# Optimization experiments

Measured on AMD Instinct MI355X. Metric: run time of the kernel, lower is better.

The kernel has to match this reference:

```python
import jax, jax.numpy as jnp
import numpy as np

B, H, W, C = 4, 128, 128, 180
NH, WS = 6, 16
HD = C // NH
SCALE = HD ** -0.5
CONV_SCALE = 0.01
CR, SQ = 3, 30
HIDDEN = int(C * 4.0)


def setup_inputs() -> dict:
    key = jax.random.key(0)
    ks = iter(jax.random.split(key, 32))
    def rn(shape, s=0.02):
        return jax.random.normal(next(ks), shape, jnp.float32) * s
    return {
        "x": jax.random.normal(next(ks), (B, H * W, C), jnp.float32),
        "rpi": jax.random.randint(next(ks), (WS * WS, WS * WS), 0, (2 * WS - 1) ** 2),
        "attn_mask": jnp.zeros((1, 1, 1), jnp.int32),
        "triangular_masks": jnp.zeros((1,), jnp.int32),
        "h": H,
        "w": W,
        "norm1_g": jnp.ones((C,), jnp.float32), "norm1_b": jnp.zeros((C,), jnp.float32),
        "qkv_w": rn((C, 3 * C)), "qkv_b": jnp.zeros((3 * C,), jnp.float32),
        "rpb": rn(((2 * WS - 1) ** 2, NH)),
        "proj_w": rn((C, C)), "proj_b": jnp.zeros((C,), jnp.float32),
        "conv1_w": rn((3, 3, C, C // CR)), "conv1_b": jnp.zeros((C // CR,), jnp.float32),
        "conv2_w": rn((3, 3, C // CR, C)), "conv2_b": jnp.zeros((C,), jnp.float32),
        "ca1_w": rn((C, C // SQ)), "ca1_b": jnp.zeros((C // SQ,), jnp.float32),
        "ca2_w": rn((C // SQ, C)), "ca2_b": jnp.zeros((C,), jnp.float32),
        "norm2_g": jnp.ones((C,), jnp.float32), "norm2_b": jnp.zeros((C,), jnp.float32),
        "fc1_w": rn((C, HIDDEN)), "fc1_b": jnp.zeros((HIDDEN,), jnp.float32),
        "fc2_w": rn((HIDDEN, C)), "fc2_b": jnp.zeros((C,), jnp.float32),
    }


def _ln(x, g, b):
    mu = jnp.mean(x, -1, keepdims=True)
    var = jnp.var(x, -1, keepdims=True)
    return (x - mu) * jax.lax.rsqrt(var + 1e-5) * g + b


def _conv(x, w, b):
    y = jax.lax.conv_general_dilated(x, w, (1, 1), 'SAME',
                                     dimension_numbers=('NHWC', 'HWIO', 'NHWC'))
    return y + b


def _forward(x, norm1_g, norm1_b, qkv_w, qkv_b, rpb, proj_w, proj_b,
             conv1_w, conv1_b, conv2_w, conv2_b, ca1_w, ca1_b, ca2_w, ca2_b,
             norm2_g, norm2_b, fc1_w, fc1_b, fc2_w, fc2_b, rpi):
    b = x.shape[0]
    shortcut = x
    xn = _ln(x, norm1_g, norm1_b).reshape(b, H, W, C)
    # ---- CAB conv branch (conv3x3 -> GELU -> conv3x3 -> channel attention) ----
    y = _conv(xn, conv1_w, conv1_b)
    y = jax.nn.gelu(y, approximate=False)
    y = _conv(y, conv2_w, conv2_b)
    pooled = jnp.mean(y, axis=(1, 2))                      # (b, C) adaptive avg pool
    a = jax.nn.relu(pooled @ ca1_w + ca1_b)
    a = jax.nn.sigmoid(a @ ca2_w + ca2_b)
    conv_x = (y * a[:, None, None, :]).reshape(b, H * W, C)
    # ---- window partition (shift_size=0, triangular_flag=0) ----
    xw = xn.reshape(b, H // WS, WS, W // WS, WS, C)
    xw = xw.transpose(0, 1, 3, 2, 4, 5).reshape(-1, WS * WS, C)  # (b_, n, C)
    b_, n = xw.shape[0], WS * WS
    # ---- W-MSA with relative position bias ----
    qkv = (xw @ qkv_w + qkv_b).reshape(b_, n, 3, NH, HD).transpose(2, 0, 3, 1, 4)
    q, k, v = qkv[0] * SCALE, qkv[1], qkv[2]               # (b_, NH, n, HD)
    attn = jnp.einsum('bhnd,bhmd->bhnm', q, k)
    bias = rpb[rpi.reshape(-1)].reshape(n, n, NH).transpose(2, 0, 1)  # (NH, n, n)
    attn = jax.nn.softmax(attn + bias[None], axis=-1)
    out = jnp.einsum('bhnm,bhmd->bhnd', attn, v)
    out = out.transpose(0, 2, 1, 3).reshape(b_, n, C) @ proj_w + proj_b
    # ---- window reverse ----
    attn_x = out.reshape(b, H // WS, W // WS, WS, WS, C)
    attn_x = attn_x.transpose(0, 1, 3, 2, 4, 5).reshape(b, H * W, C)
    x = shortcut + attn_x + conv_x * CONV_SCALE
    # ---- MLP ----
    xn2 = _ln(x, norm2_g, norm2_b)
    m = jax.nn.gelu(xn2 @ fc1_w + fc1_b, approximate=False) @ fc2_w + fc2_b
    return x + m


def reference(x, rpi, attn_mask, triangular_masks, h, w,
              norm1_g, norm1_b, qkv_w, qkv_b, rpb, proj_w, proj_b,
              conv1_w, conv1_b, conv2_w, conv2_b, ca1_w, ca1_b, ca2_w, ca2_b,
              norm2_g, norm2_b, fc1_w, fc1_b, fc2_w, fc2_b):
    # attn_mask / triangular_masks unused: shift_size=0, triangular_flag=0.
    return _forward(x, norm1_g, norm1_b, qkv_w, qkv_b, rpb, proj_w, proj_b,
                    conv1_w, conv1_b, conv2_w, conv2_b, ca1_w, ca1_b, ca2_w, ca2_b,
                    norm2_g, norm2_b, fc1_w, fc1_b, fc2_w, fc2_b, rpi)
```

## Files before the change

kernel.cpp:

```cpp
#include <hip/hip_runtime.h>
#include <hip/hip_bf16.h>
#include <math.h>

typedef __hip_bfloat16 bf16;

#define B_    4
#define C_    180
#define ROWS_ 65536
#define NH_   6
#define HD_   30
#define NT_   256
#define CC_   60
#define HID_  720
#define ATT_SCALE 0.18257418583505536f

typedef short  short4v __attribute__((ext_vector_type(4)));
typedef short  short8v __attribute__((ext_vector_type(8)));
typedef __bf16 bf16x8  __attribute__((ext_vector_type(8)));
typedef float  f32x4   __attribute__((ext_vector_type(4)));

__device__ __forceinline__ float b2f(bf16 v){ return __bfloat162float(v); }
__device__ __forceinline__ bf16  f2b(float v){ return __float2bfloat16(v); }
__device__ __forceinline__ float ldf(const bf16* p){ return __bfloat162float(*p); }
__device__ __forceinline__ float ldf(const float* p){ return *p; }
__device__ __forceinline__ float gelu_f(float v){
    return 0.5f * v * (1.0f + erff(v * 0.70710678118654752440f));
}
__device__ __forceinline__ f32x4 mfma16(short8v a, short8v b, f32x4 c){
    return __builtin_amdgcn_mfma_f32_16x16x32_bf16(
        __builtin_bit_cast(bf16x8, a), __builtin_bit_cast(bf16x8, b), c, 0, 0, 0);
}
__device__ __forceinline__ short8v cat44(short4v lo, short4v hi){
    return short8v{lo[0],lo[1],lo[2],lo[3],hi[0],hi[1],hi[2],hi[3]};
}

__device__ __forceinline__ int inv_win(int r){
    int b = r >> 14, w6 = (r >> 8) & 63, t = r & 255;
    int py = ((w6 >> 3) << 4) + (t >> 4);
    int px = ((w6 & 7) << 4) + (t & 15);
    return (b << 14) + (py << 7) + px;
}

template<typename TIN>
__global__ __launch_bounds__(256) void ln_kernel(const TIN* __restrict__ xin,
        const float* __restrict__ gw, const float* __restrict__ gb,
        bf16* __restrict__ xn)
{
    int row  = blockIdx.x * 4 + (threadIdx.x >> 6);
    int lane = threadIdx.x & 63;
    const TIN* xp = xin + (size_t)row * C_;
    float v0 = ldf(xp + lane);
    float v1 = ldf(xp + lane + 64);
    float v2 = (lane < 52) ? ldf(xp + lane + 128) : 0.f;
    float s  = v0 + v1 + v2;
    float sq = v0*v0 + v1*v1 + v2*v2;
    for (int off = 32; off > 0; off >>= 1){
        s  += __shfl_xor(s,  off);
        sq += __shfl_xor(sq, off);
    }
    float mu  = s * (1.f / 180.f);
    float inv = rsqrtf(sq * (1.f / 180.f) - mu * mu + 1e-5f);
    size_t ro = (size_t)row * C_;
    #pragma unroll
    for (int e = 0; e < 3; e++){
        int c = lane + e * 64;
        if (c < C_){
            float v = (e == 0) ? v0 : (e == 1 ? v1 : v2);
            xn[ro + c] = f2b((v - mu) * inv * gw[c] + gb[c]);
        }
    }
}

__global__ __launch_bounds__(256) void twt_kernel(const float* __restrict__ w,
        bf16* __restrict__ bt, int K, int N, int KP, int NP)
{
    int idx = blockIdx.x * 256 + threadIdx.x;
    if (idx >= NP * KP) return;
    int n = idx / KP, k = idx % KP;
    float v = (n < N && k < K) ? w[(size_t)k * N + n] : 0.f;
    bt[idx] = f2b(v);
}
__global__ __launch_bounds__(256) void twc_kernel(const float* __restrict__ w,
        bf16* __restrict__ bt, int CIN, int N, int SEGP, int NP)
{
    int KP = 9 * SEGP;
    int idx = blockIdx.x * 256 + threadIdx.x;
    if (idx >= NP * KP) return;
    int n = idx / KP, kk = idx % KP;
    int seg = kk / SEGP, ci = kk - seg * SEGP;
    float v = (n < N && ci < CIN) ? w[((size_t)seg * CIN + ci) * N + n] : 0.f;
    bt[idx] = f2b(v);
}

__global__ __launch_bounds__(192) void pool_kernel(const bf16* __restrict__ y2,
                                                   float* __restrict__ pooled)
{
    int b = blockIdx.x >> 6;
    int chunk = blockIdx.x & 63;
    int c = threadIdx.x;
    if (c >= C_) return;
    const bf16* p = y2 + ((size_t)(b << 14) + (chunk << 8)) * C_ + c;
    float s = 0.f;
    for (int i = 0; i < 256; i++) s += b2f(p[(size_t)i * C_]);
    atomicAdd(&pooled[b * C_ + c], s);
}

__global__ __launch_bounds__(192) void ca_kernel(const float* __restrict__ pooled,
        const float* __restrict__ w1, const float* __restrict__ b1,
        const float* __restrict__ w2, const float* __restrict__ b2v,
        float* __restrict__ aout)
{
    __shared__ float t[NH_];
    int b = blockIdx.x, tid = threadIdx.x;
    if (tid < 6){
        float s = b1[tid];
        for (int c = 0; c < C_; c++)
            s += pooled[b * C_ + c] * (1.f / 16384.f) * w1[c * 6 + tid];
        t[tid] = fmaxf(s, 0.f);
    }
    __syncthreads();
    if (tid < C_){
        float s = b2v[tid];
        #pragma unroll
        for (int j = 0; j < 6; j++) s += t[j] * w2[j * C_ + tid];
        aout[b * C_ + tid] = 1.f / (1.f + __expf(-s));
    }
}

__global__ __launch_bounds__(256) void rpb_kernel(const float* __restrict__ rpb,
        const int* __restrict__ rpi, bf16* __restrict__ biasT)
{
    int idx = blockIdx.x * 256 + threadIdx.x;
    int h = idx >> 16, ij = idx & 65535;
    biasT[idx] = f2b(rpb[rpi[ij] * 6 + h]);
}

template<int EPI, int MODE, int SEGP, int CSTR>
__global__ __launch_bounds__(256) void mgemm_kernel(const bf16* __restrict__ A,
        const bf16* __restrict__ BT, const float* __restrict__ bias,
        void* outp, int N, int KP, int row0, int ldA,
        const float* __restrict__ xres, const bf16* __restrict__ resb,
        const float* __restrict__ aab)
{
    __shared__ short As[2][128 * 32];
    __shared__ short Bs[2][64 * 32];
    int tid = threadIdx.x;
    int gm0 = blockIdx.x * 128;
    int n0  = blockIdx.y * 64;
    f32x4 acc[2][4];
    #pragma unroll
    for (int i = 0; i < 2; i++)
        #pragma unroll
        for (int j = 0; j < 4; j++)
            acc[i][j] = (f32x4)0.f;

    int lane = tid & 63, wv = tid >> 6;
    int quad = lane >> 4, l15 = lane & 15;
    int ar = tid >> 1, aq = (tid & 1) * 2;
    int bn = tid >> 2, bq = tid & 3;
    int nch = KP >> 5;

    auto loadA8 = [&](int kc, int s) -> short8v {
        int k0 = kc * 32;
        int gk = k0 + (aq + s) * 8;
        if (MODE == 2){
            int mg = gm0 + ar;
            int bb = mg >> 14, p = mg & 16383;
            int py = p >> 7, px = p & 127;
            int seg = k0 / SEGP;
            int kh = seg / 3, kw = seg - kh * 3;
            int ci = gk - seg * SEGP;
            int y = py + kh - 1, xx = px + kw - 1;
            if ((unsigned)y < 128u && (unsigned)xx < 128u){
                const bf16* ap = A + ((size_t)(bb << 14) + (y << 7) + xx) * CSTR + ci;
                return cat44(*(const short4v*)ap, *(const short4v*)(ap + 4));
            }
            return short8v{0,0,0,0,0,0,0,0};
        } else {
            int arow = gm0 + ar;
            if (MODE == 1) arow = inv_win(row0 + arow);
            const bf16* ap = A + (size_t)arow * ldA + gk;
            return cat44(*(const short4v*)ap, *(const short4v*)(ap + 4));
        }
    };
    auto loadB8 = [&](int kc) -> short8v {
        const bf16* bp = BT + (size_t)(n0 + bn) * KP + kc * 32 + bq * 8;
        return cat44(*(const short4v*)bp, *(const short4v*)(bp + 4));
    };
    auto storeA = [&](int buf, short8v v0, short8v v1){
        int base = ar * 32;
        int sw = (ar >> 1) & 3;
        *(short8v*)&As[buf][base + (aq ^ sw) * 8]       = v0;
        *(short8v*)&As[buf][base + ((aq + 1) ^ sw) * 8] = v1;
    };
    auto storeB = [&](int buf, short8v v){
        *(short8v*)&Bs[buf][bn * 32 + (bq ^ ((bn >> 1) & 3)) * 8] = v;
    };

    {
        short8v a0 = loadA8(0, 0), a1 = loadA8(0, 1), b0 = loadB8(0);
        storeA(0, a0, a1); storeB(0, b0);
    }
    for (int kc = 0; kc < nch; kc++){
        int cur = kc & 1;
        __syncthreads();
        short8v na0, na1, nb0;
        bool more = (kc + 1 < nch);
        if (more){ na0 = loadA8(kc + 1, 0); na1 = loadA8(kc + 1, 1); nb0 = loadB8(kc + 1); }
        short8v af[2], bfr[4];
        #pragma unroll
        for (int i = 0; i < 2; i++){
            int r = wv * 32 + i * 16 + l15;
            int pp = quad ^ ((r >> 1) & 3);
            af[i] = *(const short8v*)&As[cur][r * 32 + pp * 8];
        }
        #pragma unroll
        for (int j = 0; j < 4; j++){
            int n = j * 16 + l15;
            int pp = quad ^ ((n >> 1) & 3);
            bfr[j] = *(const short8v*)&Bs[cur][n * 32 + pp * 8];
        }
        #pragma unroll
        for (int i = 0; i < 2; i++)
            #pragma unroll
            for (int j = 0; j < 4; j++)
                acc[i][j] = mfma16(af[i], bfr[j], acc[i][j]);
        if (more){ storeA(cur ^ 1, na0, na1); storeB(cur ^ 1, nb0); }
    }

    #pragma unroll
    for (int i = 0; i < 2; i++){
        #pragma unroll
        for (int reg = 0; reg < 4; reg++){
            int gr = gm0 + wv * 32 + i * 16 + quad * 4 + reg;
            #pragma unroll
            for (int j = 0; j < 4; j++){
                int gc = n0 + j * 16 + l15;
                if (gc >= N) continue;
                float v = acc[i][j][reg] + bias[gc];
                if (EPI == 1) v = gelu_f(v);
                if (EPI == 0 || EPI == 1){
                    ((bf16*)outp)[(size_t)gr * N + gc] = f2b(v);
                } else if (EPI == 2){
                    size_t oi = (size_t)gr * N + gc;
                    ((float*)outp)[oi] = v + b2f(resb[oi]);
                } else {
                    int nr = inv_win(row0 + gr);
                    size_t oi = (size_t)nr * C_ + gc;
                    bf16* ob = (bf16*)outp;
                    v += xres[oi] + b2f(ob[oi]) * aab[(nr >> 14) * C_ + gc] * 0.01f;
                    ob[oi] = f2b(v);
                }
            }
        }
    }
}

#define KS_STR 36
#define VT_STR 260
#define P_STR  132
__global__ __launch_bounds__(256) void attn_kernel(const bf16* __restrict__ qkv,
        const bf16* __restrict__ biasT, bf16* __restrict__ attn_o)
{
    __shared__ short lds[256*KS_STR + 32*VT_STR + 64*P_STR];
    short* Ks = lds;
    short* Vt = lds + 256*KS_STR;
    bf16*  Pp = (bf16*)(lds + 256*KS_STR + 32*VT_STR);

    int tid = threadIdx.x;
    int win = blockIdx.x / NH_;
    int h   = blockIdx.x % NH_;
    const bf16* wbase = qkv + (size_t)win * NT_ * 540;

    {
        int t = tid;
        const bf16* row = wbase + (size_t)t * 540;
        const uint* kp = (const uint*)(row + 180 + h * HD_);
        const uint* vp = (const uint*)(row + 360 + h * HD_);
        uint* kd = (uint*)(Ks + t * KS_STR);
        #pragma unroll
        for (int i = 0; i < 15; i++) kd[i] = kp[i];
        kd[15] = 0; kd[16] = 0; kd[17] = 0;
        #pragma unroll
        for (int i = 0; i < 15; i++){
            uint w = vp[i];
            Vt[(2*i  ) * VT_STR + t] = (short)(w & 0xffff);
            Vt[(2*i+1) * VT_STR + t] = (short)(w >> 16);
        }
        Vt[30 * VT_STR + t] = 0;
        Vt[31 * VT_STR + t] = 0;
    }
    __syncthreads();

    int lane = tid & 63, wv = tid >> 6;
    int quad = lane >> 4, l15 = lane & 15;
    const bf16* qbase = wbase + h * HD_;
    const bf16* brow  = biasT + (size_t)h * 65536;

    for (int qb = 0; qb < 4; qb++){
        int qrow = qb * 64 + wv * 16 + l15;
        short8v af;
        {
            const uint* qp = (const uint*)(qbase + (size_t)qrow * 540 + quad * 8);
            union { uint u[4]; short8v v; } qa;
            qa.u[0] = qp[0]; qa.u[1] = qp[1]; qa.u[2] = qp[2]; qa.u[3] = qp[3];
            af = qa.v;
        }
        f32x4 Oacc[2];
        Oacc[0] = (f32x4)0.f; Oacc[1] = (f32x4)0.f;
        float lsum[4] = {0.f, 0.f, 0.f, 0.f};

        for (int kh = 0; kh < 2; kh++){
            f32x4 s[8];
            #pragma unroll
            for (int jt = 0; jt < 8; jt++) s[jt] = (f32x4)0.f;
            #pragma unroll
            for (int jt = 0; jt < 8; jt++){
                int tok = kh * 128 + jt * 16 + l15;
                const short* kp = Ks + tok * KS_STR + quad * 8;
                short8v bfr = cat44(*(const short4v*)kp, *(const short4v*)(kp + 4));
                s[jt] = mfma16(af, bfr, s[jt]);
            }
            float part[4] = {0.f, 0.f, 0.f, 0.f};
            #pragma unroll
            for (int jt = 0; jt < 8; jt++){
                int j = kh * 128 + jt * 16 + l15;
                #pragma unroll
                for (int reg = 0; reg < 4; reg++){
                    int i = qb * 64 + wv * 16 + quad * 4 + reg;
                    float v = s[jt][reg] * ATT_SCALE + b2f(brow[(size_t)i * 256 + j]);
                    float p = __expf(v);
                    part[reg] += p;
                    Pp[(wv * 16 + quad * 4 + reg) * P_STR + jt * 16 + l15] = f2b(p);
                }
            }
            #pragma unroll
            for (int m = 1; m < 16; m <<= 1){
                #pragma unroll
                for (int reg = 0; reg < 4; reg++)
                    part[reg] += __shfl_xor(part[reg], m);
            }
            #pragma unroll
            for (int reg = 0; reg < 4; reg++) lsum[reg] += part[reg];
            #pragma unroll
            for (int kc = 0; kc < 4; kc++){
                const short* pa_p = (const short*)Pp + (wv * 16 + l15) * P_STR
                                    + kc * 32 + quad * 8;
                short8v pa = cat44(*(const short4v*)pa_p, *(const short4v*)(pa_p + 4));
                #pragma unroll
                for (int jt2 = 0; jt2 < 2; jt2++){
                    const short* vb_p = Vt + (jt2 * 16 + l15) * VT_STR
                                        + kh * 128 + kc * 32 + quad * 8;
                    short8v vb = cat44(*(const short4v*)vb_p, *(const short4v*)(vb_p + 4));
                    Oacc[jt2] = mfma16(pa, vb, Oacc[jt2]);
                }
            }
        }
        #pragma unroll
        for (int jt2 = 0; jt2 < 2; jt2++){
            int d = jt2 * 16 + l15;
            if (d < HD_){
                #pragma unroll
                for (int reg = 0; reg < 4; reg++){
                    int qr = qb * 64 + wv * 16 + quad * 4 + reg;
                    attn_o[((size_t)win * NT_ + qr) * C_ + h * HD_ + d] =
                        f2b(Oacc[jt2][reg] / lsum[reg]);
                }
            }
        }
    }
}

extern "C" void kernel_launch(void* const* d_in, const int* in_sizes, int n_in,
                              void* d_out, int out_size, void* d_ws, size_t ws_size,
                              hipStream_t stream)
{
    const float* x      = (const float*)d_in[0];
    const int*   rpi    = (const int*)  d_in[1];
    const float* n1g    = (const float*)d_in[6];
    const float* n1b    = (const float*)d_in[7];
    const float* qkv_w  = (const float*)d_in[8];
    const float* qkv_b  = (const float*)d_in[9];
    const float* rpb    = (const float*)d_in[10];
    const float* proj_w = (const float*)d_in[11];
    const float* proj_b = (const float*)d_in[12];
    const float* c1w    = (const float*)d_in[13];
    const float* c1b    = (const float*)d_in[14];
    const float* c2w    = (const float*)d_in[15];
    const float* c2b    = (const float*)d_in[16];
    const float* ca1w   = (const float*)d_in[17];
    const float* ca1b   = (const float*)d_in[18];
    const float* ca2w   = (const float*)d_in[19];
    const float* ca2b   = (const float*)d_in[20];
    const float* n2g    = (const float*)d_in[21];
    const float* n2b    = (const float*)d_in[22];
    const float* fc1w   = (const float*)d_in[23];
    const float* fc1b   = (const float*)d_in[24];
    const float* fc2w   = (const float*)d_in[25];
    const float* fc2b   = (const float*)d_in[26];

    size_t fixed = 23592960ull * 2 + 786432 + 1314816 + 5760;
    int CH = (ws_size >= (size_t)32768 * 1440 + fixed) ? 2 : 4;
    int CROWS = ROWS_ / CH;
    int CWIN  = CROWS / 256;
    size_t slab_sz = (size_t)CROWS * 1440;

    char* ws = (char*)d_ws;
    bf16*  slab   = (bf16*)(ws);
    bf16*  y1     = slab;
    bf16*  qkvb   = slab;
    bf16*  attn_o = (bf16*)(ws + (size_t)CROWS * 1080);
    bf16*  hbuf   = slab;
    bf16*  xn     = (bf16*)(ws + slab_sz);
    bf16*  resbuf = (bf16*)(ws + slab_sz + 23592960);
    bf16*  biasT  = (bf16*)(ws + slab_sz + 47185920);
    bf16*  qkvT   = (bf16*)((char*)biasT + 786432);
    bf16*  projT  = (bf16*)((char*)qkvT + 221184);
    bf16*  fc1T   = (bf16*)((char*)projT + 73728);
    bf16*  fc2T   = (bf16*)((char*)fc1T + 294912);
    bf16*  c1T    = (bf16*)((char*)fc2T + 282624);
    bf16*  c2T    = (bf16*)((char*)c1T + 221184);
    float* pooled = (float*)((char*)c2T + 221184);
    float* aab    = pooled + B_ * C_;

    hipMemsetAsync(pooled, 0, B_ * C_ * sizeof(float), stream);
    rpb_kernel<<<1536, 256, 0, stream>>>(rpb, rpi, biasT);
    twt_kernel<<<(576*192+255)/256, 256, 0, stream>>>(qkv_w, qkvT, 180, 540, 192, 576);
    twt_kernel<<<(192*192+255)/256, 256, 0, stream>>>(proj_w, projT, 180, 180, 192, 192);
    twt_kernel<<<(768*192+255)/256, 256, 0, stream>>>(fc1w, fc1T, 180, 720, 192, 768);
    twt_kernel<<<(192*736+255)/256, 256, 0, stream>>>(fc2w, fc2T, 720, 180, 736, 192);
    twc_kernel<<<(64*1728+255)/256, 256, 0, stream>>>(c1w, c1T, 180, 60, 192, 64);
    twc_kernel<<<(192*576+255)/256, 256, 0, stream>>>(c2w, c2T, 60, 180, 64, 192);

    ln_kernel<float><<<16384, 256, 0, stream>>>(x, n1g, n1b, xn);

    mgemm_kernel<1, 2, 192, 180><<<dim3(512, 1), 256, 0, stream>>>(
        xn, c1T, c1b, y1, 60, 1728, 0, 0, nullptr, nullptr, nullptr);
    mgemm_kernel<0, 2, 64, 60><<<dim3(512, 3), 256, 0, stream>>>(
        y1, c2T, c2b, resbuf, 180, 576, 0, 0, nullptr, nullptr, nullptr);
    pool_kernel<<<256, 192, 0, stream>>>(resbuf, pooled);
    ca_kernel<<<4, 192, 0, stream>>>(pooled, ca1w, ca1b, ca2w, ca2b, aab);

    for (int ch = 0; ch < CH; ch++){
        int row0 = ch * CROWS;
        mgemm_kernel<0, 1, 0, 0><<<dim3(CROWS/128, 9), 256, 0, stream>>>(
            xn, qkvT, qkv_b, qkvb, 540, 192, row0, 180, nullptr, nullptr, nullptr);
        attn_kernel<<<CWIN * NH_, 256, 0, stream>>>(qkvb, biasT, attn_o);
        mgemm_kernel<3, 0, 0, 0><<<dim3(CROWS/128, 3), 256, 0, stream>>>(
            attn_o, projT, proj_b, resbuf, 180, 192, row0, 180, x, nullptr, aab);
    }

    ln_kernel<bf16><<<16384, 256, 0, stream>>>(resbuf, n2g, n2b, xn);

    for (int ch = 0; ch < CH; ch++){
        size_t off = (size_t)ch * CROWS * C_;
        mgemm_kernel<1, 0, 0, 0><<<dim3(CROWS/128, 12), 256, 0, stream>>>(
            xn + off, fc1T, fc1b, hbuf, 720, 192, 0, 180, nullptr, nullptr, nullptr);
        mgemm_kernel<2, 0, 0, 0><<<dim3(CROWS/128, 3), 256, 0, stream>>>(
            hbuf, fc2T, fc2b, (float*)d_out + off, 180, 736, 0, 720,
            nullptr, resbuf + off, nullptr);
    }
}
```

Before: 598.3 us.

## Drop LDS staging in MFMA GEMM and load fragments directly from global

```diff
diff --git a/kernel.cpp b/kernel.cpp
--- a/kernel.cpp
+++ b/kernel.cpp
@@ -32,6 +32,9 @@
 }
 __device__ __forceinline__ short8v cat44(short4v lo, short4v hi){
     return short8v{lo[0],lo[1],lo[2],lo[3],hi[0],hi[1],hi[2],hi[3]};
+}
+__device__ __forceinline__ short8v ld8(const bf16* p){
+    return cat44(*(const short4v*)p, *(const short4v*)(p + 4));
 }
 
 __device__ __forceinline__ int inv_win(int r){
@@ -135,18 +138,19 @@
     biasT[idx] = f2b(rpb[rpi[ij] * 6 + h]);
 }
 
-template<int EPI, int MODE, int SEGP, int CSTR>
-__global__ __launch_bounds__(256) void mgemm_kernel(const bf16* __restrict__ A,
+template<int EPI, int MODE, int SEGP, int CSTR, int KPT>
+__global__ __launch_bounds__(256, 4) void mgemm_kernel(const bf16* __restrict__ A,
         const bf16* __restrict__ BT, const float* __restrict__ bias,
-        void* outp, int N, int KP, int row0, int ldA,
+        void* outp, int N, int row0, int ldA,
         const float* __restrict__ xres, const bf16* __restrict__ resb,
         const float* __restrict__ aab)
 {
-    __shared__ short As[2][128 * 32];
-    __shared__ short Bs[2][64 * 32];
     int tid = threadIdx.x;
     int gm0 = blockIdx.x * 128;
     int n0  = blockIdx.y * 64;
+    int lane = tid & 63, wv = tid >> 6;
+    int quad = lane >> 4, l15 = lane & 15;
+
     f32x4 acc[2][4];
     #pragma unroll
     for (int i = 0; i < 2; i++)
@@ -154,78 +158,70 @@
         for (int j = 0; j < 4; j++)
             acc[i][j] = (f32x4)0.f;
 
-    int lane = tid & 63, wv = tid >> 6;
-    int quad = lane >> 4, l15 = lane & 15;
-    int ar = tid >> 1, aq = (tid & 1) * 2;
-    int bn = tid >> 2, bq = tid & 3;
-    int nch = KP >> 5;
-
-    auto loadA8 = [&](int kc, int s) -> short8v {
-        int k0 = kc * 32;
-        int gk = k0 + (aq + s) * 8;
-        if (MODE == 2){
-            int mg = gm0 + ar;
-            int bb = mg >> 14, p = mg & 16383;
-            int py = p >> 7, px = p & 127;
-            int seg = k0 / SEGP;
-            int kh = seg / 3, kw = seg - kh * 3;
-            int ci = gk - seg * SEGP;
-            int y = py + kh - 1, xx = px + kw - 1;
-            if ((unsigned)y < 128u && (unsigned)xx < 128u){
-                const bf16* ap = A + ((size_t)(bb << 14) + (y << 7) + xx) * CSTR + ci;
-                return cat44(*(const short4v*)ap, *(const short4v*)(ap + 4));
-            }
-            return short8v{0,0,0,0,0,0,0,0};
-        } else {
-            int arow = gm0 + ar;
-            if (MODE == 1) arow = inv_win(row0 + arow);
-            const bf16* ap = A + (size_t)arow * ldA + gk;
-            return cat44(*(const short4v*)ap, *(const short4v*)(ap + 4));
-        }
-    };
-    auto loadB8 = [&](int kc) -> short8v {
-        const bf16* bp = BT + (size_t)(n0 + bn) * KP + kc * 32 + bq * 8;
-        return cat44(*(const short4v*)bp, *(const short4v*)(bp + 4));
-    };
-    auto storeA = [&](int buf, short8v v0, short8v v1){
-        int base = ar * 32;
-        int sw = (ar >> 1) & 3;
-        *(short8v*)&As[buf][base + (aq ^ sw) * 8]       = v0;
-        *(short8v*)&As[buf][base + ((aq + 1) ^ sw) * 8] = v1;
-    };
-    auto storeB = [&](int buf, short8v v){
-        *(short8v*)&Bs[buf][bn * 32 + (bq ^ ((bn >> 1) & 3)) * 8] = v;
-    };
-
-    {
-        short8v a0 = loadA8(0, 0), a1 = loadA8(0, 1), b0 = loadB8(0);
-        storeA(0, a0, a1); storeB(0, b0);
-    }
-    for (int kc = 0; kc < nch; kc++){
-        int cur = kc & 1;
-        __syncthreads();
-        short8v na0, na1, nb0;
-        bool more = (kc + 1 < nch);
-        if (more){ na0 = loadA8(kc + 1, 0); na1 = loadA8(kc + 1, 1); nb0 = loadB8(kc + 1); }
-        short8v af[2], bfr[4];
+    const bf16* brow[4];
+    #pragma unroll
+    for (int j = 0; j < 4; j++)
+        brow[j] = BT + (size_t)(n0 + j * 16 + l15) * KPT + quad * 8;
+
+    if (MODE == 2){
+        int py[2], px[2]; size_t pbase[2];
         #pragma unroll
         for (int i = 0; i < 2; i++){
-            int r = wv * 32 + i * 16 + l15;
-            int pp = quad ^ ((r >> 1) & 3);
-            af[i] = *(const short8v*)&As[cur][r * 32 + pp * 8];
-        }
-        #pragma unroll
-        for (int j = 0; j < 4; j++){
-            int n = j * 16 + l15;
-            int pp = quad ^ ((n >> 1) & 3);
-            bfr[j] = *(const short8v*)&Bs[cur][n * 32 + pp * 8];
-        }
-        #pragma unroll
-        for (int i = 0; i < 2; i++)
-            #pragma unroll
-            for (int j = 0; j < 4; j++)
-                acc[i][j] = mfma16(af[i], bfr[j], acc[i][j]);
-        if (more){ storeA(cur ^ 1, na0, na1); storeB(cur ^ 1, nb0); }
+            int m = gm0 + wv * 32 + i * 16 + l15;
+            int bb = m >> 14, p = m & 16383;
+            py[i] = p >> 7; px[i] = p & 127;
+            pbase[i] = (size_t)bb << 14;
+        }
+        #pragma unroll
+        for (int seg = 0; seg < 9; seg++){
+            const int kh = seg / 3, kw = seg - kh * 3;
+            const bf16* ap[2]; bool val[2];
+            #pragma unroll
+            for (int i = 0; i < 2; i++){
+                int y = py[i] + kh - 1, xx = px[i] + kw - 1;
+                val[i] = ((unsigned)y < 128u) && ((unsigned)xx < 128u);
+                ap[i] = A + (pbase[i] + (size_t)(y * 128 + xx)) * CSTR + quad * 8;
+            }
+            constexpr int CIN = SEGP / 32;
+            #pragma unroll
+            for (int cc = 0; cc < CIN; cc++){
+                short8v af[2], bfr[4];
+                #pragma unroll
+                for (int i = 0; i < 2; i++)
+                    af[i] = val[i] ? ld8(ap[i] + cc * 32)
+                                   : short8v{0,0,0,0,0,0,0,0};
+                #pragma unroll
+                for (int j = 0; j < 4; j++)
+                    bfr[j] = ld8(brow[j] + seg * SEGP + cc * 32);
+                #pragma unroll
+                for (int i = 0; i < 2; i++)
+                    #pragma unroll
+                    for (int j = 0; j < 4; j++)
+                        acc[i][j] = mfma16(af[i], bfr[j], acc[i][j]);
+            }
+        }
+    } else {
+        const bf16* arp[2];
+        #pragma unroll
+        for (int i = 0; i < 2; i++){
+            int m = gm0 + wv * 32 + i * 16 + l15;
+            if (MODE == 1) m = inv_win(row0 + m);
+            arp[i] = A + (size_t)m * ldA + quad * 8;
+        }
+        constexpr int NCH = KPT / 32;
+        #pragma unroll
+        for (int kc = 0; kc < NCH; kc++){
+            short8v af[2], bfr[4];
+            #pragma unroll
+            for (int i = 0; i < 2; i++) af[i] = ld8(arp[i] + kc * 32);
+            #pragma unroll
+            for (int j = 0; j < 4; j++) bfr[j] = ld8(brow[j] + kc * 32);
+            #pragma unroll
+            for (int i = 0; i < 2; i++)
+                #pragma unroll
+                for (int j = 0; j < 4; j++)
+                    acc[i][j] = mfma16(af[i], bfr[j], acc[i][j]);
+        }
     }
 
     #pragma unroll
@@ -318,8 +314,7 @@
             for (int jt = 0; jt < 8; jt++){
                 int tok = kh * 128 + jt * 16 + l15;
                 const short* kp = Ks + tok * KS_STR + quad * 8;
-                short8v bfr = cat44(*(const short4v*)kp, *(const short4v*)(kp + 4));
-                s[jt] = mfma16(af, bfr, s[jt]);
+                s[jt] = mfma16(af, cat44(*(const short4v*)kp, *(const short4v*)(kp + 4)), s[jt]);
             }
             float part[4] = {0.f, 0.f, 0.f, 0.f};
             #pragma unroll
@@ -434,30 +429,30 @@
 
     ln_kernel<float><<<16384, 256, 0, stream>>>(x, n1g, n1b, xn);
 
-    mgemm_kernel<1, 2, 192, 180><<<dim3(512, 1), 256, 0, stream>>>(
-        xn, c1T, c1b, y1, 60, 1728, 0, 0, nullptr, nullptr, nullptr);
-    mgemm_kernel<0, 2, 64, 60><<<dim3(512, 3), 256, 0, stream>>>(
-        y1, c2T, c2b, resbuf, 180, 576, 0, 0, nullptr, nullptr, nullptr);
+    mgemm_kernel<1, 2, 192, 180, 1728><<<dim3(512, 1), 256, 0, stream>>>(
+        xn, c1T, c1b, y1, 60, 0, 180, nullptr, nullptr, nullptr);
+    mgemm_kernel<0, 2, 64, 60, 576><<<dim3(512, 3), 256, 0, stream>>>(
+        y1, c2T, c2b, resbuf, 180, 0, 60, nullptr, nullptr, nullptr);
     pool_kernel<<<256, 192, 0, stream>>>(resbuf, pooled);
     ca_kernel<<<4, 192, 0, stream>>>(pooled, ca1w, ca1b, ca2w, ca2b, aab);
 
     for (int ch = 0; ch < CH; ch++){
         int row0 = ch * CROWS;
-        mgemm_kernel<0, 1, 0, 0><<<dim3(CROWS/128, 9), 256, 0, stream>>>(
-            xn, qkvT, qkv_b, qkvb, 540, 192, row0, 180, nullptr, nullptr, nullptr);
+        mgemm_kernel<0, 1, 0, 0, 192><<<dim3(CROWS/128, 9), 256, 0, stream>>>(
+            xn, qkvT, qkv_b, qkvb, 540, row0, 180, nullptr, nullptr, nullptr);
         attn_kernel<<<CWIN * NH_, 256, 0, stream>>>(qkvb, biasT, attn_o);
-        mgemm_kernel<3, 0, 0, 0><<<dim3(CROWS/128, 3), 256, 0, stream>>>(
-            attn_o, projT, proj_b, resbuf, 180, 192, row0, 180, x, nullptr, aab);
+        mgemm_kernel<3, 0, 0, 0, 192><<<dim3(CROWS/128, 3), 256, 0, stream>>>(
+            attn_o, projT, proj_b, resbuf, 180, row0, 180, x, nullptr, aab);
     }
 
     ln_kernel<bf16><<<16384, 256, 0, stream>>>(resbuf, n2g, n2b, xn);
 
     for (int ch = 0; ch < CH; ch++){
         size_t off = (size_t)ch * CROWS * C_;
-        mgemm_kernel<1, 0, 0, 0><<<dim3(CROWS/128, 12), 256, 0, stream>>>(
-            xn + off, fc1T, fc1b, hbuf, 720, 192, 0, 180, nullptr, nullptr, nullptr);
-        mgemm_kernel<2, 0, 0, 0><<<dim3(CROWS/128, 3), 256, 0, stream>>>(
-            hbuf, fc2T, fc2b, (float*)d_out + off, 180, 736, 0, 720,
+        mgemm_kernel<1, 0, 0, 0, 192><<<dim3(CROWS/128, 12), 256, 0, stream>>>(
+            xn + off, fc1T, fc1b, hbuf, 720, 0, 180, nullptr, nullptr, nullptr);
+        mgemm_kernel<2, 0, 0, 0, 736><<<dim3(CROWS/128, 3), 256, 0, stream>>>(
+            hbuf, fc2T, fc2b, (float*)d_out + off, 180, 0, 720,
             nullptr, resbuf + off, nullptr);
     }
 }
```

New measurement: 738.6 us. 23.4% more time.
